# Kernel tuning notes

Hardware: AMD Instinct MI355X
Metric: run time of the kernel (lower is better)

The kernel has to match this reference:

```python
import jax, jax.numpy as jnp
import numpy as np

# Layer configuration (from init_kwargs)
T = 32
TSEQ = jnp.linspace(1.0 / T, 1.0, T, dtype=jnp.float32)  # tseq grid
N_HOM_DIMS = 2      # dimensions = [0, 1]
KMAX = 4            # KK = [0,1,2,3] -> top-4 landscapes

B, N, P = 128, 256 * 256, 4096  # batch, grid cells, persistence pairs


def setup_inputs() -> dict:
    key = jax.random.key(0)
    k1, k2, k3, k4 = jax.random.split(key, 4)
    fun_value = jax.random.uniform(k1, (B, N), dtype=jnp.float32)
    birth_idx = jax.random.randint(k2, (B, P), 0, N, dtype=jnp.int32)
    death_idx = jax.random.randint(k3, (B, P), 0, N, dtype=jnp.int32)
    pair_dim = jax.random.randint(k4, (B, P), 0, N_HOM_DIMS, dtype=jnp.int32)
    return {"fun_value": fun_value, "birth_idx": birth_idx,
            "death_idx": death_idx, "pair_dim": pair_dim}


def reference(fun_value, birth_idx, death_idx, pair_dim):
    # Gather birth/death filtration values of each persistence pair
    # (this is fun_value[locationBirth] / fun_value[locationDeath]).
    b = jnp.take_along_axis(fun_value, birth_idx, axis=-1)   # [B, P]
    d = jnp.take_along_axis(fun_value, death_idx, axis=-1)   # [B, P]
    # Tent functions: fab[b, t, p] = max(min(tseq[t] - birth_p, death_p - tseq[t]), 0)
    fab = jnp.maximum(
        jnp.minimum(TSEQ[None, :, None] - b[:, None, :],
                    d[:, None, :] - TSEQ[None, :, None]),
        0.0)                                                  # [B, T, P]
    # Restrict pairs to each homology dimension; out-of-dim pairs become the
    # zero padding the original code uses in its fab buffer.
    dims = jnp.arange(N_HOM_DIMS, dtype=pair_dim.dtype)
    in_dim = pair_dim[:, None, None, :] == dims[None, :, None, None]  # [B, D, 1, P]
    fab_d = jnp.where(in_dim, fab[:, None, :, :], 0.0)        # [B, D, T, P]
    # Landscape = top-KMAX values over pairs (== -sort(-fab)[..., KK]).
    land, _ = jax.lax.top_k(fab_d, KMAX)                      # [B, D, T, KMAX]
    return land
```

## Files before the change

### kernel.cpp

```cpp
#include <hip/hip_runtime.h>

#define B_ 128
#define N_ 65536
#define P_ 4096
#define T_ 32
#define D_ 2
#define K_ 4
#define S_ 16
#define PPB 256

#define INS(v0, v1, v2, v3, val)                                  \
    {                                                             \
        float _x = fminf(v0, val); v0 = fmaxf(v0, val);           \
        float _y = fminf(v1, _x);  v1 = fmaxf(v1, _x);            \
        float _z = fminf(v2, _y);  v2 = fmaxf(v2, _y);            \
        v3 = fmaxf(v3, _z);                                       \
    }

__global__ __launch_bounds__(256, 8) void fused_scan(
        const float* __restrict__ fun,
        const int* __restrict__ bidx,
        const int* __restrict__ didx,
        const int* __restrict__ pdim,
        float* __restrict__ partial) {
    __shared__ float2 bdS[PPB + 4];
    __shared__ int    cntS[4];
    __shared__ float  mrg[4][64][4];

    int bid   = blockIdx.x;
    int xcd   = bid & 7;
    int seq   = bid >> 3;
    int batch = xcd * 16 + (seq & 15);
    int slice = seq >> 4;

    int tid  = threadIdx.x;
    int lane = tid & 63;
    int wave = tid >> 6;
    int base = batch * P_ + slice * PPB;

    const float* f = fun + (size_t)batch * N_;
    int p  = base + tid;
    int pd = pdim[p];
    int bi = bidx[p];
    int di = didx[p];
    float b = f[bi];
    float d = f[di];

    unsigned long long bal = __ballot(pd == 0);
    if (lane == 0) cntS[wave] = __popcll(bal);
    __syncthreads();

    int pre0 = 0, pre1 = 0, n0tot = 0;
    #pragma unroll
    for (int s = 0; s < 4; ++s) {
        int cs = cntS[s];
        if (s < wave) { pre0 += cs; pre1 += 64 - cs; }
        n0tot += cs;
    }
    int n1tot = PPB - n0tot;
    int A   = (n0tot + 1) & ~1;
    int n1p = (n1tot + 1) & ~1;

    unsigned long long lmask = (1ull << lane) - 1ull;
    int r = __popcll(bal & lmask);
    int dst = (pd == 0) ? (pre0 + r) : (A + pre1 + (lane - r));
    bdS[dst] = make_float2(b, d);
    if (tid == 0 && (n0tot & 1)) bdS[n0tot]     = make_float2(4.f, -4.f);
    if (tid == 1 && (n1tot & 1)) bdS[A + n1tot] = make_float2(4.f, -4.f);
    __syncthreads();

    int half = lane >> 5;
    int t    = lane & 31;
    float tf = (float)(t + 1) * 0.03125f;

    float a0 = 0.f, a1 = 0.f, a2 = 0.f, a3 = 0.f;
    float c0 = 0.f, c1 = 0.f, c2 = 0.f, c3 = 0.f;

    #pragma unroll 4
    for (int j = wave * 2; j < A; j += 8) {
        float2 pr = bdS[j + half];
        float val = fminf(tf - pr.x, pr.y - tf);
        INS(a0, a1, a2, a3, val);
    }
    #pragma unroll 4
    for (int j = A + wave * 2; j < A + n1p; j += 8) {
        float2 pr = bdS[j + half];
        float val = fminf(tf - pr.x, pr.y - tf);
        INS(c0, c1, c2, c3, val);
    }

    float u0 = (half == 0) ? a0 : c0, w0 = (half == 0) ? c0 : a0;
    float u1 = (half == 0) ? a1 : c1, w1 = (half == 0) ? c1 : a1;
    float u2 = (half == 0) ? a2 : c2, w2 = (half == 0) ? c2 : a2;
    float u3 = (half == 0) ? a3 : c3, w3 = (half == 0) ? c3 : a3;
    float q;
    q = __shfl_xor(w0, 32); INS(u0, u1, u2, u3, q);
    q = __shfl_xor(w1, 32); INS(u0, u1, u2, u3, q);
    q = __shfl_xor(w2, 32); INS(u0, u1, u2, u3, q);
    q = __shfl_xor(w3, 32); INS(u0, u1, u2, u3, q);

    mrg[wave][lane][0] = u0;
    mrg[wave][lane][1] = u1;
    mrg[wave][lane][2] = u2;
    mrg[wave][lane][3] = u3;
    __syncthreads();

    if (wave == 0) {
        float v0 = 0.f, v1 = 0.f, v2 = 0.f, v3 = 0.f;
        #pragma unroll
        for (int w = 0; w < 4; ++w) {
            #pragma unroll
            for (int k = 0; k < 4; ++k) {
                float val = mrg[w][lane][k];
                INS(v0, v1, v2, v3, val);
            }
        }
        float* dstp = partial + (((size_t)batch * S_ + slice) * 64 + lane) * 4;
        dstp[0] = v0; dstp[1] = v1; dstp[2] = v2; dstp[3] = v3;
    }
}

__global__ __launch_bounds__(256) void final_merge(
        const float* __restrict__ partial,
        float* __restrict__ out) {
    int tid   = blockIdx.x * 256 + threadIdx.x;
    int batch = tid >> 6;
    int combo = tid & 63;
    float v0 = 0.f, v1 = 0.f, v2 = 0.f, v3 = 0.f;
    const float4* src = (const float4*)(partial + (((size_t)batch * S_) * 64 + combo) * 4);
    for (int s = 0; s < S_; ++s) {
        float4 val4 = src[(size_t)s * 64];
        INS(v0, v1, v2, v3, val4.x);
        INS(v1, v1, v2, v3, val4.y);
        INS(v2, v2, v3, v3, val4.z);
        v3 = v3;
    }
    v0 = v1 = v2 = v3 = 0.f;
    for (int s = 0; s < S_; ++s) {
        float4 val4 = src[(size_t)s * 64];
        INS(v0, v1, v2, v3, val4.x);
        INS(v0, v1, v2, v3, val4.y);
        INS(v0, v1, v2, v3, val4.z);
        INS(v0, v1, v2, v3, val4.w);
    }
    float* dst = out + (size_t)tid * 4;
    dst[0] = v0; dst[1] = v1; dst[2] = v2; dst[3] = v3;
}

extern "C" void kernel_launch(void* const* d_in, const int* in_sizes, int n_in,
                              void* d_out, int out_size, void* d_ws, size_t ws_size,
                              hipStream_t stream) {
    const float* fun  = (const float*)d_in[0];
    const int*   bidx = (const int*)d_in[1];
    const int*   didx = (const int*)d_in[2];
    const int*   pdim = (const int*)d_in[3];
    float* out = (float*)d_out;

    float* partial = (float*)d_ws;

    fused_scan<<<B_ * S_, 256, 0, stream>>>(fun, bidx, didx, pdim, partial);
    final_merge<<<(B_ * 64) / 256, 256, 0, stream>>>(partial, out);
}
```

Baseline: 91.90 us.

## Assign one block per batch and dimension, drop final merge kernel

Replaces the two-kernel design (16 slices per batch plus a global merge pass) with a single kernel launching one 512-thread block per (batch, homology dim). Each wave loads eight pairs per lane with int4 vector loads, keeps only pairs of its own dimension, gathers only those values, compacts them into its own shared segment, then merges per-wave top-4 in shared memory and writes the output directly. This removes the partial-buffer round trip and the second launch, and halves the gathers per block. The cost is that each pair index is read by two blocks and only 256 blocks run, which may leave much of the GPU underused.

```diff
diff --git a/kernel.cpp b/kernel.cpp
--- a/kernel.cpp
+++ b/kernel.cpp
@@ -6,8 +6,6 @@
 #define T_ 32
 #define D_ 2
 #define K_ 4
-#define S_ 16
-#define PPB 256
 
 #define INS(v0, v1, v2, v3, val)                                  \
     {                                                             \
@@ -17,134 +15,105 @@
         v3 = fmaxf(v3, _z);                                       \
     }
 
-__global__ __launch_bounds__(256, 8) void fused_scan(
+__global__ __launch_bounds__(512) void fused_pl(
         const float* __restrict__ fun,
         const int* __restrict__ bidx,
         const int* __restrict__ didx,
         const int* __restrict__ pdim,
-        float* __restrict__ partial) {
-    __shared__ float2 bdS[PPB + 4];
-    __shared__ int    cntS[4];
-    __shared__ float  mrg[4][64][4];
+        float* __restrict__ out) {
+    __shared__ float2 bdS[8][512];
+    __shared__ float  mrg[8][32][4];
 
     int bid   = blockIdx.x;
     int xcd   = bid & 7;
     int seq   = bid >> 3;
     int batch = xcd * 16 + (seq & 15);
-    int slice = seq >> 4;
+    int mydim = seq >> 4;
 
     int tid  = threadIdx.x;
     int lane = tid & 63;
     int wave = tid >> 6;
-    int base = batch * P_ + slice * PPB;
+
+    int pbase = batch * P_ + wave * 512 + lane * 8;
+    const int4* bp = (const int4*)(bidx + pbase);
+    const int4* dp = (const int4*)(didx + pbase);
+    const int4* pp = (const int4*)(pdim + pbase);
+    int4 bi0 = bp[0], bi1 = bp[1];
+    int4 di0 = dp[0], di1 = dp[1];
+    int4 pd0 = pp[0], pd1 = pp[1];
 
     const float* f = fun + (size_t)batch * N_;
-    int p  = base + tid;
-    int pd = pdim[p];
-    int bi = bidx[p];
-    int di = didx[p];
-    float b = f[bi];
-    float d = f[di];
+    float2* seg = &bdS[wave][0];
+    unsigned long long lm = (1ull << lane) - 1ull;
+    int off = 0;
 
-    unsigned long long bal = __ballot(pd == 0);
-    if (lane == 0) cntS[wave] = __popcll(bal);
-    __syncthreads();
+#define ROUND(PD, BI, DI)                                         \
+    {                                                             \
+        bool keep = ((PD) == mydim);                              \
+        unsigned long long bal = __ballot(keep);                  \
+        if (keep) {                                               \
+            int rank = __popcll(bal & lm);                        \
+            float b = f[(BI)];                                    \
+            float d = f[(DI)];                                    \
+            seg[off + rank] = make_float2(b, d);                  \
+        }                                                         \
+        off += __popcll(bal);                                     \
+    }
+    ROUND(pd0.x, bi0.x, di0.x)
+    ROUND(pd0.y, bi0.y, di0.y)
+    ROUND(pd0.z, bi0.z, di0.z)
+    ROUND(pd0.w, bi0.w, di0.w)
+    ROUND(pd1.x, bi1.x, di1.x)
+    ROUND(pd1.y, bi1.y, di1.y)
+    ROUND(pd1.z, bi1.z, di1.z)
+    ROUND(pd1.w, bi1.w, di1.w)
+#undef ROUND
 
-    int pre0 = 0, pre1 = 0, n0tot = 0;
-    #pragma unroll
-    for (int s = 0; s < 4; ++s) {
-        int cs = cntS[s];
-        if (s < wave) { pre0 += cs; pre1 += 64 - cs; }
-        n0tot += cs;
-    }
-    int n1tot = PPB - n0tot;
-    int A   = (n0tot + 1) & ~1;
-    int n1p = (n1tot + 1) & ~1;
-
-    unsigned long long lmask = (1ull << lane) - 1ull;
-    int r = __popcll(bal & lmask);
-    int dst = (pd == 0) ? (pre0 + r) : (A + pre1 + (lane - r));
-    bdS[dst] = make_float2(b, d);
-    if (tid == 0 && (n0tot & 1)) bdS[n0tot]     = make_float2(4.f, -4.f);
-    if (tid == 1 && (n1tot & 1)) bdS[A + n1tot] = make_float2(4.f, -4.f);
-    __syncthreads();
+    if (lane == 0 && (off & 1)) seg[off] = make_float2(4.f, -4.f);
+    int cnt = (off + 1) & ~1;
 
     int half = lane >> 5;
     int t    = lane & 31;
     float tf = (float)(t + 1) * 0.03125f;
 
-    float a0 = 0.f, a1 = 0.f, a2 = 0.f, a3 = 0.f;
-    float c0 = 0.f, c1 = 0.f, c2 = 0.f, c3 = 0.f;
-
+    float v0 = 0.f, v1 = 0.f, v2 = 0.f, v3 = 0.f;
     #pragma unroll 4
-    for (int j = wave * 2; j < A; j += 8) {
-        float2 pr = bdS[j + half];
+    for (int j = half; j < cnt; j += 2) {
+        float2 pr = seg[j];
         float val = fminf(tf - pr.x, pr.y - tf);
-        INS(a0, a1, a2, a3, val);
-    }
-    #pragma unroll 4
-    for (int j = A + wave * 2; j < A + n1p; j += 8) {
-        float2 pr = bdS[j + half];
-        float val = fminf(tf - pr.x, pr.y - tf);
-        INS(c0, c1, c2, c3, val);
+        INS(v0, v1, v2, v3, val);
     }
 
-    float u0 = (half == 0) ? a0 : c0, w0 = (half == 0) ? c0 : a0;
-    float u1 = (half == 0) ? a1 : c1, w1 = (half == 0) ? c1 : a1;
-    float u2 = (half == 0) ? a2 : c2, w2 = (half == 0) ? c2 : a2;
-    float u3 = (half == 0) ? a3 : c3, w3 = (half == 0) ? c3 : a3;
-    float q;
-    q = __shfl_xor(w0, 32); INS(u0, u1, u2, u3, q);
-    q = __shfl_xor(w1, 32); INS(u0, u1, u2, u3, q);
-    q = __shfl_xor(w2, 32); INS(u0, u1, u2, u3, q);
-    q = __shfl_xor(w3, 32); INS(u0, u1, u2, u3, q);
+    float m0 = __shfl_xor(v0, 32);
+    float m1 = __shfl_xor(v1, 32);
+    float m2 = __shfl_xor(v2, 32);
+    float m3 = __shfl_xor(v3, 32);
+    INS(v0, v1, v2, v3, m0);
+    INS(v0, v1, v2, v3, m1);
+    INS(v0, v1, v2, v3, m2);
+    INS(v0, v1, v2, v3, m3);
 
-    mrg[wave][lane][0] = u0;
-    mrg[wave][lane][1] = u1;
-    mrg[wave][lane][2] = u2;
-    mrg[wave][lane][3] = u3;
+    if (half == 0) {
+        mrg[wave][t][0] = v0;
+        mrg[wave][t][1] = v1;
+        mrg[wave][t][2] = v2;
+        mrg[wave][t][3] = v3;
+    }
     __syncthreads();
 
-    if (wave == 0) {
-        float v0 = 0.f, v1 = 0.f, v2 = 0.f, v3 = 0.f;
+    if (wave == 0 && half == 0) {
+        float u0 = 0.f, u1 = 0.f, u2 = 0.f, u3 = 0.f;
         #pragma unroll
-        for (int w = 0; w < 4; ++w) {
-            #pragma unroll
-            for (int k = 0; k < 4; ++k) {
-                float val = mrg[w][lane][k];
-                INS(v0, v1, v2, v3, val);
-            }
+        for (int w = 0; w < 8; ++w) {
+            float4 val4 = *(const float4*)&mrg[w][t][0];
+            INS(u0, u1, u2, u3, val4.x);
+            INS(u0, u1, u2, u3, val4.y);
+            INS(u0, u1, u2, u3, val4.z);
+            INS(u0, u1, u2, u3, val4.w);
         }
-        float* dstp = partial + (((size_t)batch * S_ + slice) * 64 + lane) * 4;
-        dstp[0] = v0; dstp[1] = v1; dstp[2] = v2; dstp[3] = v3;
+        *(float4*)(out + ((size_t)batch * 64 + mydim * 32 + t) * 4) =
+            make_float4(u0, u1, u2, u3);
     }
-}
-
-__global__ __launch_bounds__(256) void final_merge(
-        const float* __restrict__ partial,
-        float* __restrict__ out) {
-    int tid   = blockIdx.x * 256 + threadIdx.x;
-    int batch = tid >> 6;
-    int combo = tid & 63;
-    float v0 = 0.f, v1 = 0.f, v2 = 0.f, v3 = 0.f;
-    const float4* src = (const float4*)(partial + (((size_t)batch * S_) * 64 + combo) * 4);
-    for (int s = 0; s < S_; ++s) {
-        float4 val4 = src[(size_t)s * 64];
-        INS(v0, v1, v2, v3, val4.x);
-        INS(v1, v1, v2, v3, val4.y);
-        INS(v2, v2, v3, v3, val4.z);
-        v3 = v3;
-    }
-    v0 = v1 = v2 = v3 = 0.f;
-    for (int s = 0; s < S_; ++s) {
-        float4 val4 = src[(size_t)s * 64];
-        INS(v0, v1, v2, v3, val4.x);
-        INS(v0, v1, v2, v3, val4.y);
-        INS(v0, v1, v2, v3, val4.z);
-        INS(v0, v1, v2, v3, val4.w);
-    }
-    float* dst = out + (size_t)tid * 4;
-    dst[0] = v0; dst[1] = v1; dst[2] = v2; dst[3] = v3;
 }
 
 extern "C" void kernel_launch(void* const* d_in, const int* in_sizes, int n_in,
@@ -156,8 +125,5 @@
     const int*   pdim = (const int*)d_in[3];
     float* out = (float*)d_out;
 
-    float* partial = (float*)d_ws;
-
-    fused_scan<<<B_ * S_, 256, 0, stream>>>(fun, bidx, didx, pdim, partial);
-    final_merge<<<(B_ * 64) / 256, 256, 0, stream>>>(partial, out);
+    fused_pl<<<B_ * D_, 512, 0, stream>>>(fun, bidx, didx, pdim, out);
 }
```

Result: faster. 89.88 us (-2.2%).
